# Performance work log

Measured on AMD Instinct MI355X. Metric: run time of the kernel, lower is better.

The kernel has to match this reference:

```python
import jax, jax.numpy as jnp
import numpy as np

N, E, H, R, A = 100000, 1600000, 128, 500, 16  # nodes, edges, hidden, reservoir, actions
LN_EPS = 1e-5

def setup_inputs() -> dict:
    key = jax.random.key(0)
    ks = jax.random.split(key, 8)
    return {
        "node_feats": jax.random.normal(ks[0], (N, 2), jnp.float32),
        "edge_index": jax.random.randint(ks[1], (2, E), 0, N, dtype=jnp.int32),
        "esn_state": jax.random.normal(ks[2], (1, R), jnp.float32),
        "gcn_w": jax.random.normal(ks[3], (2, H), jnp.float32) * 0.5,
        "gcn_b": jnp.zeros((H,), jnp.float32),
        "ln_w": jnp.ones((H,), jnp.float32),
        "ln_b": jnp.zeros((H,), jnp.float32),
        "fc1_w": jax.random.normal(ks[4], (H + R, H), jnp.float32) * 0.04,
        "fc1_b": jnp.zeros((H,), jnp.float32),
        "fc2_w": jax.random.normal(ks[5], (H, A), jnp.float32) * 0.08,
        "fc2_b": jnp.zeros((A,), jnp.float32),
    }

def reference(node_feats, edge_index, esn_state, gcn_w, gcn_b, ln_w, ln_b,
              fc1_w, fc1_b, fc2_w, fc2_b):
    src, dst = edge_index[0], edge_index[1]
    n = node_feats.shape[0]
    # GCNConv: linear transform, then symmetric-normalized aggregation with self-loops
    h = node_feats @ gcn_w  # [N, H]
    deg = jax.ops.segment_sum(jnp.ones_like(src, dtype=h.dtype), dst, num_segments=n) + 1.0
    dis = jax.lax.rsqrt(deg)  # deg >= 1 due to self-loops
    norm = dis[src] * dis[dst]  # [E]
    agg = jax.ops.segment_sum(h[src] * norm[:, None], dst, num_segments=n)  # [N, H]
    x = agg + h * (dis * dis)[:, None] + gcn_b  # self-loop term + bias
    x = jax.nn.relu(x)
    # PyG LayerNorm, mode='graph', batch=None: normalize over all nodes & channels
    x = x - x.mean()
    x = x / (jnp.sqrt(x.var()) + LN_EPS)
    x = x * ln_w + ln_b
    pooled = x.sum(axis=0, keepdims=True)  # global_add_pool, single graph -> [1, H]
    z = jnp.concatenate([pooled, esn_state], axis=1)  # [1, H+R]
    z = jax.nn.relu(z @ fc1_w + fc1_b)
    logits = z @ fc2_w + fc2_b  # [1, A]
    return jax.nn.log_softmax(logits, axis=1)
```

## Files before the change

kernel.cpp:

```cpp
#include <hip/hip_runtime.h>
#include <math.h>

#define NN 100000
#define EE 1600000
#define HH 128
#define RR 500
#define AA 16
#define LN_EPS 1e-5f

#define BSH 8
#define NPB 256
#define NB 391
#define MAXPB 4608
#define EPW 8192
#define SCT 512
#define NWG_SC ((EE + EPW - 1) / EPW)
#define NZW 64
#define BAT 512
#define NSREP 8

__global__ __launch_bounds__(256) void k_init_esn(unsigned int* __restrict__ zero_region,
                                                  const float* __restrict__ esn,
                                                  const float* __restrict__ fc1_w,
                                                  float* __restrict__ zpart,
                                                  const float* __restrict__ fc2_w,
                                                  const float* __restrict__ ln_w,
                                                  const float* __restrict__ ln_b,
                                                  float* __restrict__ sink) {
    const int w = blockIdx.x, t = threadIdx.x;
    if (w == 0) {
        for (int j = t; j < 1545; j += 256) zero_region[j] = 0u;
        return;
    }
    if (w <= NZW) {
        const int sl = w - 1;
        const int k0 = sl * 8;
        const int k1 = min(k0 + 8, RR);
        if (t < HH) {
            float acc = 0.f;
            for (int k = k0; k < k1; ++k)
                acc = fmaf(esn[k], fc1_w[(size_t)(HH + k) * HH + t], acc);
            zpart[(size_t)sl * HH + t] = acc;
        }
        return;
    }
    if (w <= NZW + 16) {
        const int wi = w - NZW - 1;
        const float4* f4 = reinterpret_cast<const float4*>(fc1_w);
        float4 vv = f4[wi * 256 + t];
        float v = vv.x + vv.y + vv.z + vv.w;
        if ((t & 63) == 0) atomicAdd(&sink[wi], v);
        return;
    }
    {
        const float4* f2 = reinterpret_cast<const float4*>(fc2_w);
        float4 a = f2[t], b2 = f2[256 + t];
        float v = a.x + a.y + a.z + a.w + b2.x + b2.y + b2.z + b2.w;
        v += ln_w[t & (HH - 1)] + ln_b[t & (HH - 1)];
        if ((t & 63) == 0) atomicAdd(&sink[16], v);
    }
}

__global__ __launch_bounds__(SCT) void k_scatter(const int* __restrict__ src,
                                                 const int* __restrict__ dst,
                                                 unsigned int* __restrict__ gctr,
                                                 unsigned int* __restrict__ payload) {
    __shared__ unsigned int rank[512], hbase[512];
    const int t = threadIdx.x;
    rank[t] = 0u; hbase[t] = 0u;
    __syncthreads();
    const int e0 = blockIdx.x * EPW;
    const int ecnt = max(0, min(EPW, EE - e0));
    const int nv = ecnt >> 2;
    const int4* d4 = reinterpret_cast<const int4*>(dst + e0);
    const int4* s4 = reinterpret_cast<const int4*>(src + e0);

    unsigned int pw[16], pbr[16];
    bool vk[4];

    #pragma unroll
    for (int kk = 0; kk < 4; ++kk) {
        const int k = t + kk * SCT;
        vk[kk] = (k < nv);
        if (vk[kk]) {
            int4 d = d4[k];
            int4 s = s4[k];
            #define GRAB(i, SS, DD) { \
                unsigned int dd = (unsigned)(DD), ss = (unsigned)(SS); \
                unsigned int b = dd >> BSH; \
                unsigned int r = atomicAdd(&rank[b], 1u); \
                pw[kk * 4 + i]  = (ss << BSH) | (dd & (NPB - 1)); \
                pbr[kk * 4 + i] = (b << 16) | (r & 0xFFFFu); }
            GRAB(0, s.x, d.x) GRAB(1, s.y, d.y) GRAB(2, s.z, d.z) GRAB(3, s.w, d.w)
            #undef GRAB
        }
    }
    __syncthreads();

    if (t < NB && rank[t] > 0u) hbase[t] = atomicAdd(&gctr[t], rank[t]);
    __syncthreads();

    #pragma unroll
    for (int kk = 0; kk < 4; ++kk) {
        if (vk[kk]) {
            #define PUT(i) { \
                unsigned int b = pbr[kk * 4 + i] >> 16; \
                unsigned int slot = hbase[b] + (pbr[kk * 4 + i] & 0xFFFFu); \
                if (slot < MAXPB) payload[(size_t)b * MAXPB + slot] = pw[kk * 4 + i]; }
            PUT(0) PUT(1) PUT(2) PUT(3)
            #undef PUT
        }
    }
}

__global__ __launch_bounds__(1024) void k_bdeg_g(const unsigned int* __restrict__ gctr,
                                                 const unsigned int* __restrict__ payload,
                                                 const float* __restrict__ nf,
                                                 float* __restrict__ rsv, float* __restrict__ g) {
    __shared__ unsigned int hist[NPB];
    const int b = blockIdx.x, t = threadIdx.x;
    if (t < NPB) hist[t] = 0u;
    __syncthreads();
    const unsigned int cnt = min(gctr[b], (unsigned int)MAXPB);
    const unsigned int* pl = payload + (size_t)b * MAXPB;
    const uint4* pl4 = reinterpret_cast<const uint4*>(pl);
    const unsigned int nv = cnt >> 2;
    for (unsigned int k = t; k < nv; k += 1024) {
        uint4 p = pl4[k];
        atomicAdd(&hist[p.x & (NPB - 1)], 1u);
        atomicAdd(&hist[p.y & (NPB - 1)], 1u);
        atomicAdd(&hist[p.z & (NPB - 1)], 1u);
        atomicAdd(&hist[p.w & (NPB - 1)], 1u);
    }
    for (unsigned int k = (nv << 2) + t; k < cnt; k += 1024)
        atomicAdd(&hist[pl[k] & (NPB - 1)], 1u);
    __syncthreads();
    if (t < NPB) {
        int node = (b << BSH) + t;
        if (node < NN) {
            float df = 1.0f + (float)hist[t];
            float rs = rsqrtf(df);
            rsv[node] = rs;
            float2 f = *reinterpret_cast<const float2*>(&nf[2 * node]);
            float2 gv; gv.x = rs * f.x; gv.y = rs * f.y;
            *reinterpret_cast<float2*>(&g[2 * node]) = gv;
        }
    }
}

__global__ __launch_bounds__(BAT) void k_bagg_node(const unsigned int* __restrict__ gctr,
        const unsigned int* __restrict__ payload,
        const float* __restrict__ g, const float* __restrict__ rsv,
        const float* __restrict__ gcn_w, const float* __restrict__ gcn_b,
        float* __restrict__ S8, float* __restrict__ T2_8, unsigned int* __restrict__ done,
        const float* __restrict__ zpart,
        const float* __restrict__ ln_w, const float* __restrict__ ln_b,
        const float* __restrict__ fc1_w, const float* __restrict__ fc1_b,
        const float* __restrict__ fc2_w, const float* __restrict__ fc2_b,
        float* __restrict__ out) {
    __shared__ union {
        struct { float agg[NPB * 2]; float shSf[HH]; float shw[8]; } ba;
        struct { float psum[4][HH]; float pooled[HH]; float z[HH];
                 float logits[AA]; float red[2]; float t2s[NSREP]; } fin;
    } u;
    __shared__ int s_last;
    const int b = blockIdx.x, t = threadIdx.x;
    u.ba.agg[t] = 0.f;
    if (t < HH) u.ba.shSf[t] = 0.f;
    __syncthreads();
    const unsigned int cnt = min(gctr[b], (unsigned int)MAXPB);
    const unsigned int* pl = payload + (size_t)b * MAXPB;
    const uint4* pl4 = reinterpret_cast<const uint4*>(pl);
    const unsigned int nv = cnt >> 2;

    #define ACC(P) { \
        unsigned int s_ = (P) >> BSH, dl_ = (P) & (NPB - 1); \
        float2 gv_ = *reinterpret_cast<const float2*>(&g[2 * s_]); \
        atomicAdd(&u.ba.agg[dl_],       gv_.x); \
        atomicAdd(&u.ba.agg[NPB + dl_], gv_.y); }

    {
        const unsigned int k1 = t, k2 = t + BAT;
        uint4 p1, p2;
        const bool v1 = k1 < nv, v2 = k2 < nv;
        if (v1) p1 = pl4[k1];
        if (v2) p2 = pl4[k2];
        if (v1) { ACC(p1.x) ACC(p1.y) ACC(p1.z) ACC(p1.w) }
        if (v2) { ACC(p2.x) ACC(p2.y) ACC(p2.z) ACC(p2.w) }
    }
    for (unsigned int k = t + 2 * BAT; k < nv; k += BAT) {
        uint4 p = pl4[k];
        ACC(p.x) ACC(p.y) ACC(p.z) ACC(p.w)
    }
    for (unsigned int k = (nv << 2) + t; k < cnt; k += BAT) {
        unsigned int p = pl[k];
        ACC(p)
    }
    #undef ACC
    __syncthreads();

    const int nvalid = min(NPB, NN - (b << BSH));
    if (t < nvalid) {
        int node = (b << BSH) + t;
        float rs = rsv[node];
        float2 gv = *reinterpret_cast<const float2*>(&g[2 * node]);
        u.ba.agg[t]       = rs * (u.ba.agg[t]       + gv.x);
        u.ba.agg[NPB + t] = rs * (u.ba.agg[NPB + t] + gv.y);
    }
    __syncthreads();

    const int ch = t & (HH - 1), slot = t >> 7;
    {
        const float w0 = gcn_w[ch], w1 = gcn_w[HH + ch], bb = gcn_b[ch];
        float accS = 0.f, accT2 = 0.f;
        for (int j = slot; j < nvalid; j += 4) {
            float x = fmaf(u.ba.agg[j], w0, fmaf(u.ba.agg[NPB + j], w1, bb));
            float r = fmaxf(x, 0.f);
            accS  += r;
            accT2 += r * r;
        }
        atomicAdd(&u.ba.shSf[ch], accS);
        float v = accT2;
        for (int o = 32; o; o >>= 1) v += __shfl_down(v, o, 64);
        if ((t & 63) == 0) u.ba.shw[t >> 6] = v;
        __syncthreads();
        const int rep = b & (NSREP - 1);
        if (t < HH) atomicAdd(&S8[rep * HH + t], u.ba.shSf[t]);
        if (t == 0) {
            float s2 = 0.f;
            #pragma unroll
            for (int w = 0; w < 8; ++w) s2 += u.ba.shw[w];
            atomicAdd(&T2_8[rep], s2);
        }
    }
    __syncthreads();
    if (t == 0) {
        unsigned int old = atomicAdd(done, 1u);
        s_last = (old == NB - 1) ? 1 : 0;
    }
    __syncthreads();
    if (!s_last) return;

    const int sl = t >> 7;
    if (t < NSREP)
        u.fin.t2s[t] = __hip_atomic_load(&T2_8[t], __ATOMIC_RELAXED, __HIP_MEMORY_SCOPE_AGENT);
    if (t < HH) {
        float s = 0.f;
        #pragma unroll
        for (int r = 0; r < NSREP; ++r)
            s += __hip_atomic_load(&S8[r * HH + t], __ATOMIC_RELAXED, __HIP_MEMORY_SCOPE_AGENT);
        u.fin.pooled[t] = s;
        float vv = s;
        for (int o = 32; o; o >>= 1) vv += __shfl_down(vv, o, 64);
        if ((t & 63) == 0) u.fin.red[t >> 6] = vv;
    }
    __syncthreads();
    const float T1 = u.fin.red[0] + u.fin.red[1];
    float T2v = 0.f;
    #pragma unroll
    for (int r = 0; r < NSREP; ++r) T2v += u.fin.t2s[r];
    const float cntf = (float)NN * (float)HH;
    const float mean = T1 / cntf;
    const float var  = T2v / cntf - mean * mean;
    const float denom = sqrtf(var) + LN_EPS;
    if (t < HH)
        u.fin.pooled[t] = ln_w[t] * (u.fin.pooled[t] - (float)NN * mean) / denom + (float)NN * ln_b[t];
    __syncthreads();

    float acc = 0.f;
    for (int k = sl * 32; k < sl * 32 + 32; ++k)
        acc = fmaf(u.fin.pooled[k], fc1_w[(size_t)k * HH + ch], acc);
    for (int w = sl * 16; w < sl * 16 + 16; ++w)
        acc += zpart[(size_t)w * HH + ch];
    u.fin.psum[sl][ch] = acc;
    __syncthreads();
    if (t < HH) {
        float a = fc1_b[t];
        #pragma unroll
        for (int k = 0; k < 4; ++k) a += u.fin.psum[k][t];
        u.fin.z[t] = fmaxf(a, 0.f);
    }
    __syncthreads();

    if (t < AA) {
        float l = fc2_b[t];
        for (int j = 0; j < HH; ++j)
            l = fmaf(u.fin.z[j], fc2_w[j * AA + t], l);
        u.fin.logits[t] = l;
    }
    __syncthreads();

    if (t == 0) {
        float m = u.fin.logits[0];
        for (int a = 1; a < AA; ++a) m = fmaxf(m, u.fin.logits[a]);
        float sum = 0.f;
        for (int a = 0; a < AA; ++a) sum += expf(u.fin.logits[a] - m);
        float lse = m + logf(sum);
        for (int a = 0; a < AA; ++a) out[a] = u.fin.logits[a] - lse;
    }
}


__global__ void k_initf(unsigned int* __restrict__ p, int n) {
    int i = blockIdx.x * blockDim.x + threadIdx.x;
    int stride = gridDim.x * blockDim.x;
    for (int j = i; j < n; j += stride) p[j] = 0u;
}

__global__ void k_deg1(const int* __restrict__ dst, int* __restrict__ deg, int e) {
    int i = blockIdx.x * blockDim.x + threadIdx.x;
    if (i < e) atomicAdd(&deg[dst[i]], 1);
}

__global__ void k_g1(const int* __restrict__ deg, const float* __restrict__ nf,
                     float* __restrict__ degf, float* __restrict__ g, int n) {
    int i = blockIdx.x * blockDim.x + threadIdx.x;
    if (i < n) {
        float df = (float)(1 + deg[i]);
        degf[i] = df;
        float rs = rsqrtf(df);
        float2 f = *reinterpret_cast<const float2*>(&nf[2 * i]);
        float2 gv; gv.x = rs * f.x; gv.y = rs * f.y;
        *reinterpret_cast<float2*>(&g[2 * i]) = gv;
    }
}

__global__ void k_edge1(const int* __restrict__ src, const int* __restrict__ dst,
                        const float* __restrict__ g, float* __restrict__ B, int e) {
    int i = blockIdx.x * blockDim.x + threadIdx.x;
    if (i < e) {
        int s = src[i], d = dst[i];
        float2 gv = *reinterpret_cast<const float2*>(&g[2 * s]);
        atomicAdd(&B[2 * d],     gv.x);
        atomicAdd(&B[2 * d + 1], gv.y);
    }
}

__global__ void k_node(const float* __restrict__ nf, const float* __restrict__ degf,
                       const float* __restrict__ B,
                       const float* __restrict__ gcn_w, const float* __restrict__ gcn_b,
                       float* __restrict__ S, float* __restrict__ T2, int n) {
    const int ch   = threadIdx.x & (HH - 1);
    const int slot = threadIdx.x >> 7;
    const float w0 = gcn_w[ch];
    const float w1 = gcn_w[HH + ch];
    const float b  = gcn_b[ch];
    float accS = 0.f, accT2 = 0.f;
    for (int i = blockIdx.x * 2 + slot; i < n; i += gridDim.x * 2) {
        float df   = degf[i];
        float invd = 1.0f / df;
        float rs   = rsqrtf(df);
        float2 bv = *reinterpret_cast<const float2*>(&B[2 * i]);
        float2 f  = *reinterpret_cast<const float2*>(&nf[2 * i]);
        float b0 = rs * bv.x + f.x * invd;
        float b1 = rs * bv.y + f.y * invd;
        float xv = fmaf(b0, w0, fmaf(b1, w1, b));
        float r  = fmaxf(xv, 0.f);
        accS  += r;
        accT2 += r * r;
    }
    __shared__ float shS[HH];
    if (slot == 1) shS[ch] = accS;
    __syncthreads();
    if (slot == 0) atomicAdd(&S[ch], accS + shS[ch]);
    float v = accT2;
    for (int o = 32; o; o >>= 1) v += __shfl_down(v, o, 64);
    __shared__ float shw[4];
    if ((threadIdx.x & 63) == 0) shw[threadIdx.x >> 6] = v;
    __syncthreads();
    if (threadIdx.x == 0) atomicAdd(T2, shw[0] + shw[1] + shw[2] + shw[3]);
}

__global__ void k_final(const float* __restrict__ S, const float* __restrict__ T2ptr,
                        const float* __restrict__ esn,
                        const float* __restrict__ ln_w, const float* __restrict__ ln_b,
                        const float* __restrict__ fc1_w, const float* __restrict__ fc1_b,
                        const float* __restrict__ fc2_w, const float* __restrict__ fc2_b,
                        float* __restrict__ out) {
    const int t = threadIdx.x;
    __shared__ float sh_pooled[HH];
    __shared__ float sh_z[HH];
    __shared__ float sh_logits[AA];
    __shared__ float shred[2];

    float s = S[t];
    float v = s;
    for (int o = 32; o; o >>= 1) v += __shfl_down(v, o, 64);
    if ((t & 63) == 0) shred[t >> 6] = v;
    __syncthreads();
    const float T1 = shred[0] + shred[1];
    const float T2 = *T2ptr;
    const float cnt = (float)NN * (float)HH;
    const float mean = T1 / cnt;
    const float var  = T2 / cnt - mean * mean;
    const float denom = sqrtf(var) + LN_EPS;
    sh_pooled[t] = ln_w[t] * (s - (float)NN * mean) / denom + (float)NN * ln_b[t];
    __syncthreads();

    float acc = fc1_b[t];
    for (int k = 0; k < HH; ++k)
        acc = fmaf(sh_pooled[k], fc1_w[k * HH + t], acc);
    for (int k = 0; k < RR; ++k)
        acc = fmaf(esn[k], fc1_w[(HH + k) * HH + t], acc);
    sh_z[t] = fmaxf(acc, 0.f);
    __syncthreads();

    if (t < AA) {
        float l = fc2_b[t];
        for (int j = 0; j < HH; ++j)
            l = fmaf(sh_z[j], fc2_w[j * AA + t], l);
        sh_logits[t] = l;
    }
    __syncthreads();

    if (t == 0) {
        float m = sh_logits[0];
        for (int a = 1; a < AA; ++a) m = fmaxf(m, sh_logits[a]);
        float sum = 0.f;
        for (int a = 0; a < AA; ++a) sum += expf(sh_logits[a] - m);
        float lse = m + logf(sum);
        for (int a = 0; a < AA; ++a) out[a] = sh_logits[a] - lse;
    }
}

extern "C" void kernel_launch(void* const* d_in, const int* in_sizes, int n_in,
                              void* d_out, int out_size, void* d_ws, size_t ws_size,
                              hipStream_t stream) {
    const float* nf     = (const float*)d_in[0];
    const int*   ei     = (const int*)d_in[1];
    const float* esn    = (const float*)d_in[2];
    const float* gcn_w  = (const float*)d_in[3];
    const float* gcn_b  = (const float*)d_in[4];
    const float* ln_w   = (const float*)d_in[5];
    const float* ln_b   = (const float*)d_in[6];
    const float* fc1_w  = (const float*)d_in[7];
    const float* fc1_b  = (const float*)d_in[8];
    const float* fc2_w  = (const float*)d_in[9];
    const float* fc2_b  = (const float*)d_in[10];
    float* out = (float*)d_out;
    float* ws  = (float*)d_ws;

    const size_t OFF_S8      = 512;
    const size_t OFF_T28     = OFF_S8 + NSREP * HH;
    const size_t OFF_DONE    = OFF_T28 + NSREP;
    const size_t OFF_SINK    = 1548;
    const size_t OFF_ZPART   = 1612;
    const size_t OFF_PAYLOAD = OFF_ZPART + (size_t)NZW * HH;
    const size_t OFF_RSV     = OFF_PAYLOAD + (size_t)NB * MAXPB;
    const size_t OFF_G       = OFF_RSV + NN;
    const size_t NEED_BKT    = (OFF_G + 2 * (size_t)NN) * 4;

    if (ws_size >= NEED_BKT) {
        unsigned int* gctr    = (unsigned int*)ws;
        float*        S8      = ws + OFF_S8;
        float*        T2_8    = ws + OFF_T28;
        unsigned int* done    = (unsigned int*)ws + OFF_DONE;
        float*        sink    = ws + OFF_SINK;
        float*        zpart   = ws + OFF_ZPART;
        unsigned int* payload = (unsigned int*)ws + OFF_PAYLOAD;
        float*        rsv     = ws + OFF_RSV;
        float*        g       = ws + OFF_G;

        hipLaunchKernelGGL(k_init_esn,  dim3(NZW + 18), dim3(256),  0, stream,
                           (unsigned int*)ws, esn, fc1_w, zpart, fc2_w, ln_w, ln_b, sink);
        hipLaunchKernelGGL(k_scatter,   dim3(NWG_SC),   dim3(SCT),  0, stream, ei, ei + EE, gctr, payload);
        hipLaunchKernelGGL(k_bdeg_g,    dim3(NB),       dim3(1024), 0, stream, gctr, payload, nf, rsv, g);
        hipLaunchKernelGGL(k_bagg_node, dim3(NB),       dim3(BAT),  0, stream,
                           gctr, payload, g, rsv, gcn_w, gcn_b, S8, T2_8, done, zpart,
                           ln_w, ln_b, fc1_w, fc1_b, fc2_w, fc2_b, out);
    } else {
        int*   deg  = (int*)ws;
        float* B    = ws + NN;
        float* S    = ws + 3 * (size_t)NN;
        float* T2   = ws + 3 * (size_t)NN + 128;
        float* degf = ws + 3 * (size_t)NN + 130;
        float* g    = ws + 4 * (size_t)NN + 130;
        const int eb = (EE + 255) / 256;
        const int nb = (NN + 255) / 256;
        hipLaunchKernelGGL(k_initf, dim3(2048), dim3(256), 0, stream, (unsigned int*)ws, 3 * NN + 129);
        hipLaunchKernelGGL(k_deg1,  dim3(eb),   dim3(256), 0, stream, ei + EE, deg, EE);
        hipLaunchKernelGGL(k_g1,    dim3(nb),   dim3(256), 0, stream, deg, nf, degf, g, NN);
        hipLaunchKernelGGL(k_edge1, dim3(eb),   dim3(256), 0, stream, ei, ei + EE, g, B, EE);
        hipLaunchKernelGGL(k_node,  dim3(512),  dim3(256), 0, stream, nf, degf, B, gcn_w, gcn_b, S, T2, NN);
        hipLaunchKernelGGL(k_final, dim3(1),    dim3(128), 0, stream,
                           S, T2, esn, ln_w, ln_b, fc1_w, fc1_b, fc2_w, fc2_b, out);
    }
}
```

Measured before the change: 66.46 us.

## Replace last-block tail with two separate tail kernels and algebraic fc1 split

Removes the atomic done-counter last-block pattern from the aggregation kernel and moves the LayerNorm+fc1+fc2 tail into two new kernels. The first spreads the fc1 product over 16 blocks, precomputing pooled-sum, ln_w and ln_b contractions so normalization can be applied afterwards algebraically. The ESN partial product now uses 16 blocks of 32 rows instead of 64 blocks of 8, and the cache-prewarming sink blocks are dropped. This trades an in-kernel serialized tail for two extra kernel launches.

```diff
diff --git a/kernel.cpp b/kernel.cpp
--- a/kernel.cpp
+++ b/kernel.cpp
@@ -15,49 +15,28 @@
 #define EPW 8192
 #define SCT 512
 #define NWG_SC ((EE + EPW - 1) / EPW)
-#define NZW 64
+#define NZW 16
 #define BAT 512
 #define NSREP 8
+#define NTW 16
 
 __global__ __launch_bounds__(256) void k_init_esn(unsigned int* __restrict__ zero_region,
                                                   const float* __restrict__ esn,
                                                   const float* __restrict__ fc1_w,
-                                                  float* __restrict__ zpart,
-                                                  const float* __restrict__ fc2_w,
-                                                  const float* __restrict__ ln_w,
-                                                  const float* __restrict__ ln_b,
-                                                  float* __restrict__ sink) {
+                                                  float* __restrict__ zpart) {
     const int w = blockIdx.x, t = threadIdx.x;
     if (w == 0) {
-        for (int j = t; j < 1545; j += 256) zero_region[j] = 0u;
+        for (int j = t; j < 1544; j += 256) zero_region[j] = 0u;
         return;
     }
-    if (w <= NZW) {
-        const int sl = w - 1;
-        const int k0 = sl * 8;
-        const int k1 = min(k0 + 8, RR);
-        if (t < HH) {
-            float acc = 0.f;
-            for (int k = k0; k < k1; ++k)
-                acc = fmaf(esn[k], fc1_w[(size_t)(HH + k) * HH + t], acc);
-            zpart[(size_t)sl * HH + t] = acc;
-        }
-        return;
-    }
-    if (w <= NZW + 16) {
-        const int wi = w - NZW - 1;
-        const float4* f4 = reinterpret_cast<const float4*>(fc1_w);
-        float4 vv = f4[wi * 256 + t];
-        float v = vv.x + vv.y + vv.z + vv.w;
-        if ((t & 63) == 0) atomicAdd(&sink[wi], v);
-        return;
-    }
-    {
-        const float4* f2 = reinterpret_cast<const float4*>(fc2_w);
-        float4 a = f2[t], b2 = f2[256 + t];
-        float v = a.x + a.y + a.z + a.w + b2.x + b2.y + b2.z + b2.w;
-        v += ln_w[t & (HH - 1)] + ln_b[t & (HH - 1)];
-        if ((t & 63) == 0) atomicAdd(&sink[16], v);
+    const int sl = w - 1;
+    const int k0 = sl * 32;
+    const int k1 = min(k0 + 32, RR);
+    if (t < HH) {
+        float acc = 0.f;
+        for (int k = k0; k < k1; ++k)
+            acc = fmaf(esn[k], fc1_w[(size_t)(HH + k) * HH + t], acc);
+        zpart[(size_t)sl * HH + t] = acc;
     }
 }
 
@@ -152,21 +131,13 @@
         const unsigned int* __restrict__ payload,
         const float* __restrict__ g, const float* __restrict__ rsv,
         const float* __restrict__ gcn_w, const float* __restrict__ gcn_b,
-        float* __restrict__ S8, float* __restrict__ T2_8, unsigned int* __restrict__ done,
-        const float* __restrict__ zpart,
-        const float* __restrict__ ln_w, const float* __restrict__ ln_b,
-        const float* __restrict__ fc1_w, const float* __restrict__ fc1_b,
-        const float* __restrict__ fc2_w, const float* __restrict__ fc2_b,
-        float* __restrict__ out) {
-    __shared__ union {
-        struct { float agg[NPB * 2]; float shSf[HH]; float shw[8]; } ba;
-        struct { float psum[4][HH]; float pooled[HH]; float z[HH];
-                 float logits[AA]; float red[2]; float t2s[NSREP]; } fin;
-    } u;
-    __shared__ int s_last;
+        float* __restrict__ S8, float* __restrict__ T2_8) {
+    __shared__ float agg[NPB * 2];
+    __shared__ float shSf[HH];
+    __shared__ float shw[8];
     const int b = blockIdx.x, t = threadIdx.x;
-    u.ba.agg[t] = 0.f;
-    if (t < HH) u.ba.shSf[t] = 0.f;
+    agg[t] = 0.f;
+    if (t < HH) shSf[t] = 0.f;
     __syncthreads();
     const unsigned int cnt = min(gctr[b], (unsigned int)MAXPB);
     const unsigned int* pl = payload + (size_t)b * MAXPB;
@@ -176,8 +147,8 @@
     #define ACC(P) { \
         unsigned int s_ = (P) >> BSH, dl_ = (P) & (NPB - 1); \
         float2 gv_ = *reinterpret_cast<const float2*>(&g[2 * s_]); \
-        atomicAdd(&u.ba.agg[dl_],       gv_.x); \
-        atomicAdd(&u.ba.agg[NPB + dl_], gv_.y); }
+        atomicAdd(&agg[dl_],       gv_.x); \
+        atomicAdd(&agg[NPB + dl_], gv_.y); }
 
     {
         const unsigned int k1 = t, k2 = t + BAT;
@@ -204,99 +175,128 @@
         int node = (b << BSH) + t;
         float rs = rsv[node];
         float2 gv = *reinterpret_cast<const float2*>(&g[2 * node]);
-        u.ba.agg[t]       = rs * (u.ba.agg[t]       + gv.x);
-        u.ba.agg[NPB + t] = rs * (u.ba.agg[NPB + t] + gv.y);
+        agg[t]       = rs * (agg[t]       + gv.x);
+        agg[NPB + t] = rs * (agg[NPB + t] + gv.y);
     }
     __syncthreads();
 
     const int ch = t & (HH - 1), slot = t >> 7;
-    {
-        const float w0 = gcn_w[ch], w1 = gcn_w[HH + ch], bb = gcn_b[ch];
-        float accS = 0.f, accT2 = 0.f;
-        for (int j = slot; j < nvalid; j += 4) {
-            float x = fmaf(u.ba.agg[j], w0, fmaf(u.ba.agg[NPB + j], w1, bb));
-            float r = fmaxf(x, 0.f);
-            accS  += r;
-            accT2 += r * r;
-        }
-        atomicAdd(&u.ba.shSf[ch], accS);
-        float v = accT2;
-        for (int o = 32; o; o >>= 1) v += __shfl_down(v, o, 64);
-        if ((t & 63) == 0) u.ba.shw[t >> 6] = v;
-        __syncthreads();
-        const int rep = b & (NSREP - 1);
-        if (t < HH) atomicAdd(&S8[rep * HH + t], u.ba.shSf[t]);
-        if (t == 0) {
-            float s2 = 0.f;
-            #pragma unroll
-            for (int w = 0; w < 8; ++w) s2 += u.ba.shw[w];
-            atomicAdd(&T2_8[rep], s2);
-        }
-    }
-    __syncthreads();
+    const float w0 = gcn_w[ch], w1 = gcn_w[HH + ch], bb = gcn_b[ch];
+    float accS = 0.f, accT2 = 0.f;
+    for (int j = slot; j < nvalid; j += 4) {
+        float x = fmaf(agg[j], w0, fmaf(agg[NPB + j], w1, bb));
+        float r = fmaxf(x, 0.f);
+        accS  += r;
+        accT2 += r * r;
+    }
+    atomicAdd(&shSf[ch], accS);
+    float v = accT2;
+    for (int o = 32; o; o >>= 1) v += __shfl_down(v, o, 64);
+    if ((t & 63) == 0) shw[t >> 6] = v;
+    __syncthreads();
+    const int rep = b & (NSREP - 1);
+    if (t < HH) atomicAdd(&S8[rep * HH + t], shSf[t]);
     if (t == 0) {
-        unsigned int old = atomicAdd(done, 1u);
-        s_last = (old == NB - 1) ? 1 : 0;
-    }
-    __syncthreads();
-    if (!s_last) return;
-
-    const int sl = t >> 7;
-    if (t < NSREP)
-        u.fin.t2s[t] = __hip_atomic_load(&T2_8[t], __ATOMIC_RELAXED, __HIP_MEMORY_SCOPE_AGENT);
-    if (t < HH) {
+        float s2 = 0.f;
+        #pragma unroll
+        for (int w = 0; w < 8; ++w) s2 += shw[w];
+        atomicAdd(&T2_8[rep], s2);
+    }
+}
+
+__global__ __launch_bounds__(128) void k_tail1(const float* __restrict__ S8,
+                                               const float* __restrict__ ln_w,
+                                               const float* __restrict__ ln_b,
+                                               const float* __restrict__ fc1_w,
+                                               float* __restrict__ upart,
+                                               float* __restrict__ c1part,
+                                               float* __restrict__ c2part) {
+    const int i = blockIdx.x, t = threadIdx.x;
+    __shared__ float sh_sw[8], sh_lw[8], sh_lb[8];
+    if (t < 8) {
+        const int k = i * 8 + t;
         float s = 0.f;
         #pragma unroll
-        for (int r = 0; r < NSREP; ++r)
-            s += __hip_atomic_load(&S8[r * HH + t], __ATOMIC_RELAXED, __HIP_MEMORY_SCOPE_AGENT);
-        u.fin.pooled[t] = s;
-        float vv = s;
-        for (int o = 32; o; o >>= 1) vv += __shfl_down(vv, o, 64);
-        if ((t & 63) == 0) u.fin.red[t >> 6] = vv;
-    }
-    __syncthreads();
-    const float T1 = u.fin.red[0] + u.fin.red[1];
+        for (int r = 0; r < NSREP; ++r) s += S8[r * HH + k];
+        float lw = ln_w[k];
+        sh_sw[t] = lw * s;
+        sh_lw[t] = lw;
+        sh_lb[t] = ln_b[k];
+    }
+    __syncthreads();
+    float u = 0.f, c1 = 0.f, c2 = 0.f;
+    #pragma unroll
+    for (int kk = 0; kk < 8; ++kk) {
+        float w = fc1_w[(size_t)(i * 8 + kk) * HH + t];
+        u  = fmaf(sh_sw[kk], w, u);
+        c1 = fmaf(sh_lw[kk], w, c1);
+        c2 = fmaf(sh_lb[kk], w, c2);
+    }
+    upart[(size_t)i * HH + t]  = u;
+    c1part[(size_t)i * HH + t] = c1;
+    c2part[(size_t)i * HH + t] = c2;
+}
+
+__global__ __launch_bounds__(128) void k_tail2(const float* __restrict__ S8,
+                                               const float* __restrict__ T2_8,
+                                               const float* __restrict__ upart,
+                                               const float* __restrict__ c1part,
+                                               const float* __restrict__ c2part,
+                                               const float* __restrict__ zpart,
+                                               const float* __restrict__ fc1_b,
+                                               const float* __restrict__ fc2_w,
+                                               const float* __restrict__ fc2_b,
+                                               float* __restrict__ out) {
+    const int t = threadIdx.x;
+    __shared__ float sh_z[HH], sh_logits[AA], shred[2], sh_t2[8];
+
+    float s = 0.f;
+    #pragma unroll
+    for (int r = 0; r < NSREP; ++r) s += S8[r * HH + t];
+    float vv = s;
+    for (int o = 32; o; o >>= 1) vv += __shfl_down(vv, o, 64);
+    if ((t & 63) == 0) shred[t >> 6] = vv;
+    if (t < 8) sh_t2[t] = T2_8[t];
+    __syncthreads();
+
+    const float T1 = shred[0] + shred[1];
     float T2v = 0.f;
     #pragma unroll
-    for (int r = 0; r < NSREP; ++r) T2v += u.fin.t2s[r];
+    for (int r = 0; r < 8; ++r) T2v += sh_t2[r];
     const float cntf = (float)NN * (float)HH;
     const float mean = T1 / cntf;
     const float var  = T2v / cntf - mean * mean;
     const float denom = sqrtf(var) + LN_EPS;
-    if (t < HH)
-        u.fin.pooled[t] = ln_w[t] * (u.fin.pooled[t] - (float)NN * mean) / denom + (float)NN * ln_b[t];
-    __syncthreads();
-
-    float acc = 0.f;
-    for (int k = sl * 32; k < sl * 32 + 32; ++k)
-        acc = fmaf(u.fin.pooled[k], fc1_w[(size_t)k * HH + ch], acc);
-    for (int w = sl * 16; w < sl * 16 + 16; ++w)
-        acc += zpart[(size_t)w * HH + ch];
-    u.fin.psum[sl][ch] = acc;
-    __syncthreads();
-    if (t < HH) {
-        float a = fc1_b[t];
-        #pragma unroll
-        for (int k = 0; k < 4; ++k) a += u.fin.psum[k][t];
-        u.fin.z[t] = fmaxf(a, 0.f);
-    }
+    const float inv_denom = 1.0f / denom;
+    const float nmean = (float)NN * mean;
+
+    float u = 0.f, c1 = 0.f, c2 = 0.f, zs = 0.f;
+    #pragma unroll
+    for (int i = 0; i < NTW; ++i) {
+        u  += upart[(size_t)i * HH + t];
+        c1 += c1part[(size_t)i * HH + t];
+        c2 += c2part[(size_t)i * HH + t];
+        zs += zpart[(size_t)i * HH + t];
+    }
+    float fc1p = (u - nmean * c1) * inv_denom + (float)NN * c2;
+    sh_z[t] = fmaxf(fc1p + zs + fc1_b[t], 0.f);
     __syncthreads();
 
     if (t < AA) {
         float l = fc2_b[t];
         for (int j = 0; j < HH; ++j)
-            l = fmaf(u.fin.z[j], fc2_w[j * AA + t], l);
-        u.fin.logits[t] = l;
+            l = fmaf(sh_z[j], fc2_w[j * AA + t], l);
+        sh_logits[t] = l;
     }
     __syncthreads();
 
     if (t == 0) {
-        float m = u.fin.logits[0];
-        for (int a = 1; a < AA; ++a) m = fmaxf(m, u.fin.logits[a]);
+        float m = sh_logits[0];
+        for (int a = 1; a < AA; ++a) m = fmaxf(m, sh_logits[a]);
         float sum = 0.f;
-        for (int a = 0; a < AA; ++a) sum += expf(u.fin.logits[a] - m);
+        for (int a = 0; a < AA; ++a) sum += expf(sh_logits[a] - m);
         float lse = m + logf(sum);
-        for (int a = 0; a < AA; ++a) out[a] = u.fin.logits[a] - lse;
+        for (int a = 0; a < AA; ++a) out[a] = sh_logits[a] - lse;
     }
 }
 
@@ -442,9 +442,10 @@
 
     const size_t OFF_S8      = 512;
     const size_t OFF_T28     = OFF_S8 + NSREP * HH;
-    const size_t OFF_DONE    = OFF_T28 + NSREP;
-    const size_t OFF_SINK    = 1548;
-    const size_t OFF_ZPART   = 1612;
+    const size_t OFF_UPART   = OFF_T28 + 8;
+    const size_t OFF_C1      = OFF_UPART + (size_t)NTW * HH;
+    const size_t OFF_C2      = OFF_C1 + (size_t)NTW * HH;
+    const size_t OFF_ZPART   = OFF_C2 + (size_t)NTW * HH;
     const size_t OFF_PAYLOAD = OFF_ZPART + (size_t)NZW * HH;
     const size_t OFF_RSV     = OFF_PAYLOAD + (size_t)NB * MAXPB;
     const size_t OFF_G       = OFF_RSV + NN;
@@ -454,20 +455,24 @@
         unsigned int* gctr    = (unsigned int*)ws;
         float*        S8      = ws + OFF_S8;
         float*        T2_8    = ws + OFF_T28;
-        unsigned int* done    = (unsigned int*)ws + OFF_DONE;
-        float*        sink    = ws + OFF_SINK;
+        float*        upart   = ws + OFF_UPART;
+        float*        c1part  = ws + OFF_C1;
+        float*        c2part  = ws + OFF_C2;
         float*        zpart   = ws + OFF_ZPART;
         unsigned int* payload = (unsigned int*)ws + OFF_PAYLOAD;
         float*        rsv     = ws + OFF_RSV;
         float*        g       = ws + OFF_G;
 
-        hipLaunchKernelGGL(k_init_esn,  dim3(NZW + 18), dim3(256),  0, stream,
-                           (unsigned int*)ws, esn, fc1_w, zpart, fc2_w, ln_w, ln_b, sink);
-        hipLaunchKernelGGL(k_scatter,   dim3(NWG_SC),   dim3(SCT),  0, stream, ei, ei + EE, gctr, payload);
-        hipLaunchKernelGGL(k_bdeg_g,    dim3(NB),       dim3(1024), 0, stream, gctr, payload, nf, rsv, g);
-        hipLaunchKernelGGL(k_bagg_node, dim3(NB),       dim3(BAT),  0, stream,
-                           gctr, payload, g, rsv, gcn_w, gcn_b, S8, T2_8, done, zpart,
-                           ln_w, ln_b, fc1_w, fc1_b, fc2_w, fc2_b, out);
+        hipLaunchKernelGGL(k_init_esn,  dim3(NZW + 1), dim3(256),  0, stream,
+                           (unsigned int*)ws, esn, fc1_w, zpart);
+        hipLaunchKernelGGL(k_scatter,   dim3(NWG_SC),  dim3(SCT),  0, stream, ei, ei + EE, gctr, payload);
+        hipLaunchKernelGGL(k_bdeg_g,    dim3(NB),      dim3(1024), 0, stream, gctr, payload, nf, rsv, g);
+        hipLaunchKernelGGL(k_bagg_node, dim3(NB),      dim3(BAT),  0, stream,
+                           gctr, payload, g, rsv, gcn_w, gcn_b, S8, T2_8);
+        hipLaunchKernelGGL(k_tail1,     dim3(NTW),     dim3(128),  0, stream,
+                           S8, ln_w, ln_b, fc1_w, upart, c1part, c2part);
+        hipLaunchKernelGGL(k_tail2,     dim3(1),       dim3(128),  0, stream,
+                           S8, T2_8, upart, c1part, c2part, zpart, fc1_b, fc2_w, fc2_b, out);
     } else {
         int*   deg  = (int*)ws;
         float* B    = ws + NN;
```

Measured after the change: 68.74 us. +3.4%, slower.
